# Kernel optimization log

Hardware: AMD Instinct MI355X
Metric: run time of the kernel (lower is better)

The kernel has to match this reference:

```python
import jax, jax.numpy as jnp
import numpy as np

BETA = 0.9
THRESH = 1.0
ALPHA = 2.0  # snntorch ATan surrogate default

@jax.custom_vjp
def atan_spike(x):
    return (x > 0).astype(x.dtype)

def _atan_fwd(x):
    return atan_spike(x), x

def _atan_bwd(x, g):
    # d/dx of snntorch ATan surrogate: (alpha/2) / (1 + (pi/2*alpha*x)^2)
    return (g * (ALPHA / 2) / (1 + (jnp.pi / 2 * ALPHA * x) ** 2),)

atan_spike.defvjp(_atan_fwd, _atan_bwd)

def setup_inputs() -> dict:
    key = jax.random.key(0)
    k1, k2, k3, k4, k5 = jax.random.split(key, 5)
    B, T, F, H, O = 256, 1024, 64, 512, 64
    x = jax.random.normal(k1, (B, T, F), dtype=jnp.float32)
    s_in = 1.0 / np.sqrt(F)
    s_out = 1.0 / np.sqrt(H)
    W_in = jax.random.uniform(k2, (H, F), jnp.float32, -s_in, s_in)
    b_in = jax.random.uniform(k3, (H,), jnp.float32, -s_in, s_in)
    W_out = jax.random.uniform(k4, (O, H), jnp.float32, -s_out, s_out)
    b_out = jax.random.uniform(k5, (O,), jnp.float32, -s_out, s_out)
    return {"x": x, "W_in": W_in, "b_in": b_in, "W_out": W_out, "b_out": b_out}

def reference(x, W_in, b_in, W_out, b_out):
    B, T, F = x.shape
    H = W_in.shape[0]
    O = W_out.shape[0]
    dt = x.dtype
    # precompute input currents for all steps: [T, B, H]
    cur1_all = jnp.einsum('btf,hf->tbh', x, W_in) + b_in

    def step(carry, cur1):
        mem1, mem_out = carry
        # snntorch Leaky(subtract): reset from previous mem (detached),
        # then mem = beta*mem + input - reset*threshold, spike from new mem.
        reset1 = jax.lax.stop_gradient((mem1 > THRESH).astype(dt))
        mem1 = BETA * mem1 + cur1 - reset1 * THRESH
        spk1 = atan_spike(mem1 - THRESH)
        cur_out = spk1 @ W_out.T + b_out
        reset_o = jax.lax.stop_gradient((mem_out > THRESH).astype(dt))
        mem_out = BETA * mem_out + cur_out - reset_o * THRESH
        spk_out = atan_spike(mem_out - THRESH)
        return (mem1, mem_out), (mem_out, spk_out)

    init = (jnp.zeros((B, H), dt), jnp.zeros((B, O), dt))
    _, (mem_rec, spk_rec) = jax.lax.scan(step, init, cur1_all)
    # [T, B, O] -> [B, T, O]
    return mem_rec.transpose(1, 0, 2), spk_rec.transpose(1, 0, 2)
```

## Files before the change

kernel.cpp:

```cpp
#include <hip/hip_runtime.h>


namespace {
constexpr int kB = 256;
constexpr int kT = 1024;
constexpr int kF = 64;
constexpr int kH = 512;
constexpr int kO = 64;
constexpr float kBeta = 0.9f;
constexpr float kThresh = 1.0f;
}

typedef __attribute__((ext_vector_type(16))) float f32x16;

#define PIN8(p)                                                            \
  asm volatile("" : "+v"((p)[0]), "+v"((p)[1]), "+v"((p)[2]),              \
                    "+v"((p)[3]), "+v"((p)[4]), "+v"((p)[5]),              \
                    "+v"((p)[6]), "+v"((p)[7]))

#define BARRIER() asm volatile("s_waitcnt lgkmcnt(0)\n\ts_barrier" ::: "memory")

#define SX(i) ((i) < 16 ? sx0[(i)] : (i) < 32 ? sx1[(i)-16]                \
             : (i) < 48 ? sx2[(i)-32] : sx3[(i)-48])
#define AQ(q)                                                              \
  c0 = fmaf(SX(4*(q)+0), w[4*(q)+0], c0);                                  \
  c1 = fmaf(SX(4*(q)+1), w[4*(q)+1], c1);                                  \
  c2 = fmaf(SX(4*(q)+2), w[4*(q)+2], c2);                                  \
  c3 = fmaf(SX(4*(q)+3), w[4*(q)+3], c3);

__global__ __launch_bounds__(512)
void snn_curA(const float* __restrict__ x, const float* __restrict__ W_in,
              const float* __restrict__ b_in, float* __restrict__ cur1,
              int t0, int ntc, int l2ntc, int rpb) {
  const int l = threadIdx.x & 63;
  const int s = threadIdx.x >> 6;
  const int h = s * 64 + l;

  float w[64];
  {
    const float4* wiv = reinterpret_cast<const float4*>(W_in) + h * 16;
#pragma unroll
    for (int q = 0; q < 16; ++q) {
      const float4 v = wiv[q];
      w[4*q+0] = v.x; w[4*q+1] = v.y; w[4*q+2] = v.z; w[4*q+3] = v.w;
    }
  }
  float binh = b_in[h];
  PIN8(w + 0);  PIN8(w + 8);  PIN8(w + 16); PIN8(w + 24);
  PIN8(w + 32); PIN8(w + 40); PIN8(w + 48); PIN8(w + 56);
  asm volatile("" : "+v"(binh));

  const int row0 = blockIdx.x * rpb;
#pragma unroll 1
  for (int r = 0; r < rpb; ++r) {
    const int row = row0 + r;
    const int b = row >> l2ntc;
    const int tc = row & (ntc - 1);
    const float* xp = x + ((size_t)b * kT + (size_t)(t0 + tc)) * kF;
    f32x16 sx0, sx1, sx2, sx3;
    asm volatile("s_load_dwordx16 %0, %4, 0x0\n\t"
                 "s_load_dwordx16 %1, %4, 0x40\n\t"
                 "s_load_dwordx16 %2, %4, 0x80\n\t"
                 "s_load_dwordx16 %3, %4, 0xc0"
                 : "=&s"(sx0), "=&s"(sx1), "=&s"(sx2), "=&s"(sx3)
                 : "s"(xp));
    asm volatile("s_waitcnt lgkmcnt(0)"
                 : "+s"(sx0), "+s"(sx1), "+s"(sx2), "+s"(sx3) :: "memory");
    float c0 = binh, c1 = 0.0f, c2 = 0.0f, c3 = 0.0f;
    AQ(0) AQ(1) AQ(2) AQ(3) AQ(4) AQ(5) AQ(6) AQ(7)
    AQ(8) AQ(9) AQ(10) AQ(11) AQ(12) AQ(13) AQ(14) AQ(15)
    cur1[(size_t)row * kH + h] = (c0 + c1) + (c2 + c3);
  }
}

#define BSTEP(fk, tt)                                                      \
  do {                                                                     \
    mem1 = kBeta * mem1 + (fk) - rst1;                                     \
    const bool pr = mem1 > kThresh;                                        \
    rst1 = pr ? 1.0f : 0.0f;                                               \
    cp[(size_t)(tt) * kH] = rst1;          \
    const int tn_ = ((tt) + 8 < ntc) ? (tt) + 8 : ntc - 1;                 \
    fk = cp[(size_t)tn_ * kH];         \
  } while (0)

__global__ __launch_bounds__(512)
void snn_scanB(float* __restrict__ cs, float* __restrict__ state,
               int t0, int ntc) {
  const int b = blockIdx.x;
  const int h = threadIdx.x;
  float* m1s = state;
  float* r1s = state + kB * kH;
  const int idx = b * kH + h;
  float mem1 = 0.0f, rst1 = 0.0f;
  if (t0 != 0) { mem1 = m1s[idx]; rst1 = r1s[idx]; }

  float* cp = cs + (size_t)b * ntc * kH + h;
  float f0 = cp[0 * (size_t)kH], f1 = cp[1 * (size_t)kH];
  float f2 = cp[2 * (size_t)kH], f3 = cp[3 * (size_t)kH];
  float f4 = cp[4 * (size_t)kH], f5 = cp[5 * (size_t)kH];
  float f6 = cp[6 * (size_t)kH], f7 = cp[7 * (size_t)kH];

#pragma unroll 1
  for (int t = 0; t < ntc; t += 8) {
    BSTEP(f0, t + 0); BSTEP(f1, t + 1); BSTEP(f2, t + 2); BSTEP(f3, t + 3);
    BSTEP(f4, t + 4); BSTEP(f5, t + 5); BSTEP(f6, t + 6); BSTEP(f7, t + 7);
  }
  m1s[idx] = mem1;
  r1s[idx] = rst1;
}

#define SPK(vv, k)                                                         \
  __int_as_float(__builtin_amdgcn_readlane(__float_as_int(vv), (k)))

#define CROW(vv, rr)                                                       \
  do {                                                                     \
    float a0 = 0.0f, a1 = 0.0f, a2 = 0.0f, a3 = 0.0f;                      \
    _Pragma("unroll") for (int q = 0; q < 16; ++q) {                       \
      a0 = fmaf(SPK(vv, 4 * q + 0), wout[4 * q + 0], a0);                  \
      a1 = fmaf(SPK(vv, 4 * q + 1), wout[4 * q + 1], a1);                  \
      a2 = fmaf(SPK(vv, 4 * q + 2), wout[4 * q + 2], a2);                  \
      a3 = fmaf(SPK(vv, 4 * q + 3), wout[4 * q + 3], a3);                  \
    }                                                                      \
    red[buf][rr][s][o] = (a0 + a1) + (a2 + a3);                            \
  } while (0)

__global__ __launch_bounds__(512)
void snn_coutC(const float* __restrict__ spk, const float* __restrict__ W_out,
               const float* __restrict__ b_out, float* __restrict__ cout,
               int ntc) {
  const int j = threadIdx.x;
  const int o = j & 63;
  const int s = j >> 6;
  const size_t row0 = (size_t)blockIdx.x * 64;

  __shared__ float red[2][8][8][64];

  float wout[64];
  {
    const float4* wov =
        reinterpret_cast<const float4*>(W_out) + o * (kH / 4) + s * 16;
#pragma unroll
    for (int q = 0; q < 16; ++q) {
      const float4 v = wov[q];
      wout[4*q+0] = v.x; wout[4*q+1] = v.y;
      wout[4*q+2] = v.z; wout[4*q+3] = v.w;
    }
  }
  float bout = b_out[o];
  PIN8(wout + 0);  PIN8(wout + 8);  PIN8(wout + 16); PIN8(wout + 24);
  PIN8(wout + 32); PIN8(wout + 40); PIN8(wout + 48); PIN8(wout + 56);
  asm volatile("" : "+v"(bout));

  const float* sb = spk + row0 * kH + j;

#pragma unroll 1
  for (int rb = 0; rb < 64; rb += 8) {
    const int buf = (rb >> 3) & 1;
    float p0 = sb[(size_t)(rb + 0) * kH], p1 = sb[(size_t)(rb + 1) * kH];
    float p2 = sb[(size_t)(rb + 2) * kH], p3 = sb[(size_t)(rb + 3) * kH];
    float p4 = sb[(size_t)(rb + 4) * kH], p5 = sb[(size_t)(rb + 5) * kH];
    float p6 = sb[(size_t)(rb + 6) * kH], p7 = sb[(size_t)(rb + 7) * kH];

    CROW(p0, 0); CROW(p1, 1); CROW(p2, 2); CROW(p3, 3);
    CROW(p4, 4); CROW(p5, 5); CROW(p6, 6); CROW(p7, 7);

    BARRIER();

    float co = bout;
    co += red[buf][s][0][o]; co += red[buf][s][1][o];
    co += red[buf][s][2][o]; co += red[buf][s][3][o];
    co += red[buf][s][4][o]; co += red[buf][s][5][o];
    co += red[buf][s][6][o]; co += red[buf][s][7][o];
    cout[(row0 + (size_t)(rb + s)) * kO + o] = co;
  }
}

#define DSTEP(gk, tt)                                                      \
  do {                                                                     \
    memo = kBeta * memo + (gk) - rsto;                                     \
    const float so = (memo > kThresh) ? 1.0f : 0.0f;                       \
    rsto = so;                                                             \
    om[(size_t)(tt) * kO] = memo;                                          \
    os[(size_t)(tt) * kO] = so;                                            \
    const int tn_ = ((tt) + 8 < ntc) ? (tt) + 8 : ntc - 1;                 \
    gk = dp[(size_t)tn_ * kO];                                             \
  } while (0)

__global__ __launch_bounds__(64)
void snn_memoD(const float* __restrict__ cout, float* __restrict__ out,
               float* __restrict__ state, int t0, int ntc) {
  const int b = blockIdx.x;
  const int o = threadIdx.x;
  float* mos = state + 2 * kB * kH;
  float* ros = mos + kB * kO;
  const int idx = b * kO + o;
  float memo = 0.0f, rsto = 0.0f;
  if (t0 != 0) { memo = mos[idx]; rsto = ros[idx]; }

  const float* dp = cout + (size_t)b * ntc * kO + o;
  float* om = out + ((size_t)b * kT + t0) * kO + o;
  float* os = om + (size_t)kB * kT * kO;

  float g0 = dp[0 * (size_t)kO], g1 = dp[1 * (size_t)kO];
  float g2 = dp[2 * (size_t)kO], g3 = dp[3 * (size_t)kO];
  float g4 = dp[4 * (size_t)kO], g5 = dp[5 * (size_t)kO];
  float g6 = dp[6 * (size_t)kO], g7 = dp[7 * (size_t)kO];

#pragma unroll 1
  for (int t = 0; t < ntc; t += 8) {
    DSTEP(g0, t + 0); DSTEP(g1, t + 1); DSTEP(g2, t + 2); DSTEP(g3, t + 3);
    DSTEP(g4, t + 4); DSTEP(g5, t + 5); DSTEP(g6, t + 6); DSTEP(g7, t + 7);
  }
  mos[idx] = memo;
  ros[idx] = rsto;
}

__global__ __launch_bounds__(256)
void warm_x_kernel(const float4* __restrict__ p, int n4) {
  float acc = 0.0f;
  for (int i = blockIdx.x * blockDim.x + threadIdx.x; i < n4;
       i += gridDim.x * blockDim.x) {
    const float4 v = p[i];
    acc += v.x + v.y + v.z + v.w;
  }
  asm volatile("" ::"v"(acc));
}

__global__ __launch_bounds__(512)
__attribute__((amdgpu_waves_per_eu(2, 2)))
void snn_fused5(const float* __restrict__ x, const float* __restrict__ W_in,
                const float* __restrict__ b_in,
                const float* __restrict__ W_out,
                const float* __restrict__ b_out, float* __restrict__ out) {
  const int b = blockIdx.x;
  const int j = threadIdx.x;
  const int o = j & 63;
  const int s = j >> 6;
  __shared__ float red[2][8][64];
  float win[kF];
  {
    const float4* wiv = reinterpret_cast<const float4*>(W_in) + j * 16;
#pragma unroll
    for (int q = 0; q < 16; ++q) {
      const float4 v = wiv[q];
      win[4 * q] = v.x; win[4 * q + 1] = v.y;
      win[4 * q + 2] = v.z; win[4 * q + 3] = v.w;
    }
  }
  float wout[64];
  {
    const float4* wov =
        reinterpret_cast<const float4*>(W_out) + o * 128 + s * 16;
#pragma unroll
    for (int q = 0; q < 16; ++q) {
      const float4 v = wov[q];
      wout[4 * q] = v.x; wout[4 * q + 1] = v.y;
      wout[4 * q + 2] = v.z; wout[4 * q + 3] = v.w;
    }
  }
  float bin_j = b_in[j];
  float bout_o = b_out[o];
  PIN8(win + 0);  PIN8(win + 8);  PIN8(win + 16); PIN8(win + 24);
  PIN8(win + 32); PIN8(win + 40); PIN8(win + 48); PIN8(win + 56);
  PIN8(wout + 0);  PIN8(wout + 8);  PIN8(wout + 16); PIN8(wout + 24);
  PIN8(wout + 32); PIN8(wout + 40); PIN8(wout + 48); PIN8(wout + 56);
  asm volatile("" : "+v"(bin_j), "+v"(bout_o));
  float mem1 = 0.0f, rst1 = 0.0f, memo = 0.0f, rsto = 0.0f;
  unsigned long long mask = 0ull;
  const float4* xv = reinterpret_cast<const float4*>(x + (size_t)b * kT * kF);
  float* out_mem = out + (size_t)b * kT * kO + o;
  float* out_spk = out_mem + (size_t)kB * kT * kO;
  float4 x0, x1, x2, x3, x4, x5, x6, x7, x8, x9, x10, x11, x12, x13, x14, x15;
#define LOADX(tt)                                                          \
  do {                                                                     \
    const float4* xp = xv + (size_t)(tt) * 16;                             \
    x0 = xp[0]; x1 = xp[1]; x2 = xp[2]; x3 = xp[3];                        \
    x4 = xp[4]; x5 = xp[5]; x6 = xp[6]; x7 = xp[7];                        \
    x8 = xp[8]; x9 = xp[9]; x10 = xp[10]; x11 = xp[11];                    \
    x12 = xp[12]; x13 = xp[13]; x14 = xp[14]; x15 = xp[15];                \
  } while (0)
#define L1Q(q)                                                             \
  c0 = fmaf(x##q.x, win[4 * q + 0], c0);                                   \
  c1 = fmaf(x##q.y, win[4 * q + 1], c1);                                   \
  c2 = fmaf(x##q.z, win[4 * q + 2], c2);                                   \
  c3 = fmaf(x##q.w, win[4 * q + 3], c3);
#define LAYER1F()                                                          \
  do {                                                                     \
    float c0 = bin_j, c1 = 0.0f, c2 = 0.0f, c3 = 0.0f;                     \
    L1Q(0) L1Q(1) L1Q(2) L1Q(3) L1Q(4) L1Q(5) L1Q(6) L1Q(7)                \
    L1Q(8) L1Q(9) L1Q(10) L1Q(11) L1Q(12) L1Q(13) L1Q(14) L1Q(15)          \
    const float cur1v = (c0 + c1) + (c2 + c3);                             \
    mem1 = kBeta * mem1 + cur1v - rst1;                                    \
    const bool p = mem1 > kThresh;                                         \
    mask = __ballot(p);                                                    \
    rst1 = p ? 1.0f : 0.0f;                                                \
  } while (0)
#define L2QS(q)                                                            \
  {                                                                        \
    const float f0 = ((mlo >> (4 * (q) + 0)) & 1u) ? 1.0f : 0.0f;          \
    const float f1 = ((mlo >> (4 * (q) + 1)) & 1u) ? 1.0f : 0.0f;          \
    const float f2 = ((mlo >> (4 * (q) + 2)) & 1u) ? 1.0f : 0.0f;          \
    const float f3 = ((mlo >> (4 * (q) + 3)) & 1u) ? 1.0f : 0.0f;          \
    a0 = fmaf(f0, wout[4 * (q) + 0], a0);                                  \
    a1 = fmaf(f1, wout[4 * (q) + 1], a1);                                  \
    a2 = fmaf(f2, wout[4 * (q) + 2], a2);                                  \
    a3 = fmaf(f3, wout[4 * (q) + 3], a3);                                  \
  }
#define L2E(acc, q, i)                                                     \
  acc = acc + __uint_as_float(                                             \
      (unsigned)__builtin_amdgcn_sbfe((int)vmhi, 4 * (q) + (i)-32, 1) &    \
      __float_as_uint(wout[4 * (q) + (i)]));
#define L2QV(q)                                                            \
  { L2E(a0, q, 0) L2E(a1, q, 1) L2E(a2, q, 2) L2E(a3, q, 3) }
#define LAYER2F(buf)                                                       \
  do {                                                                     \
    const unsigned mlo = (unsigned)mask;                                   \
    unsigned vmhi = (unsigned)(mask >> 32);                                \
    asm volatile("" : "+v"(vmhi));                                         \
    float a0 = 0.0f, a1 = 0.0f, a2 = 0.0f, a3 = 0.0f;                      \
    L2QS(0) L2QS(1) L2QS(2) L2QS(3) L2QS(4) L2QS(5) L2QS(6) L2QS(7)        \
    L2QV(8) L2QV(9) L2QV(10) L2QV(11) L2QV(12) L2QV(13) L2QV(14) L2QV(15)  \
    red[(buf)][s][o] = (a0 + a1) + (a2 + a3);                              \
  } while (0)
  LOADX(0);
  LAYER1F();
  LOADX(1);
  for (int t = 1; t < kT; ++t) {
    LAYER2F((t - 1) & 1);
    BARRIER();
    float r0, r1, r2, r3, r4, r5, r6, r7;
    const int buf = (t - 1) & 1;
    if (s == 0) {
      r0 = red[buf][0][o]; r1 = red[buf][1][o];
      r2 = red[buf][2][o]; r3 = red[buf][3][o];
      r4 = red[buf][4][o]; r5 = red[buf][5][o];
      r6 = red[buf][6][o]; r7 = red[buf][7][o];
    }
    LAYER1F();
    const int tn = (t + 1 < kT) ? (t + 1) : (kT - 1);
    LOADX(tn);
    if (s == 0) {
      float co = bout_o;
      co += r0; co += r1; co += r2; co += r3;
      co += r4; co += r5; co += r6; co += r7;
      memo = kBeta * memo + co - rsto;
      const float so = (memo > kThresh) ? 1.0f : 0.0f;
      rsto = so;
      out_mem[(t - 1) * kO] = memo;
      out_spk[(t - 1) * kO] = so;
    }
  }
  LAYER2F((kT - 1) & 1);
  BARRIER();
  if (s == 0) {
    const int buf = (kT - 1) & 1;
    float co = bout_o;
    co += red[buf][0][o]; co += red[buf][1][o];
    co += red[buf][2][o]; co += red[buf][3][o];
    co += red[buf][4][o]; co += red[buf][5][o];
    co += red[buf][6][o]; co += red[buf][7][o];
    memo = kBeta * memo + co - rsto;
    const float so = (memo > kThresh) ? 1.0f : 0.0f;
    out_mem[(kT - 1) * kO] = memo;
    out_spk[(kT - 1) * kO] = so;
  }
}

extern "C" void kernel_launch(void* const* d_in, const int* in_sizes, int n_in,
                              void* d_out, int out_size, void* d_ws,
                              size_t ws_size, hipStream_t stream) {
  const float* x = (const float*)d_in[0];
  const float* W_in = (const float*)d_in[1];
  const float* b_in = (const float*)d_in[2];
  const float* W_out = (const float*)d_in[3];
  const float* b_out = (const float*)d_in[4];
  float* out = (float*)d_out;

  const size_t state_bytes = ((size_t)2 * kB * kH + 2 * kB * kO) * 4;
  int nch = 0;
  for (int c : {4, 8, 16}) {
    const int ntc_c = kT / c;
    const size_t need = (size_t)kB * ntc_c * (kH + kO) * 4 + state_bytes;
    if (need <= ws_size) { nch = c; break; }
  }

  if (nch) {
    const int ntc = kT / nch;
    const int l2ntc = (ntc == 256) ? 8 : (ntc == 128) ? 7 : 6;
    float* cur1 = (float*)d_ws;
    float* coutb = cur1 + (size_t)kB * ntc * kH;
    float* state = coutb + (size_t)kB * ntc * kO;

    const int rows = kB * ntc;
    const int rpbA = 128;
    const int gA = rows / rpbA;
    const int gC = rows / 64;

    for (int c = 0; c < nch; ++c) {
      const int t0 = c * ntc;
      hipLaunchKernelGGL(snn_curA, dim3(gA), dim3(512), 0, stream,
                         x, W_in, b_in, cur1, t0, ntc, l2ntc, rpbA);
      hipLaunchKernelGGL(snn_scanB, dim3(kB), dim3(512), 0, stream,
                         cur1, state, t0, ntc);
      hipLaunchKernelGGL(snn_coutC, dim3(gC), dim3(512), 0, stream,
                         cur1, W_out, b_out, coutb, ntc);
      hipLaunchKernelGGL(snn_memoD, dim3(kB), dim3(64), 0, stream,
                         coutb, out, state, t0, ntc);
    }
  } else {
    const int n4 = kB * kT * kF / 4;
    hipLaunchKernelGGL(warm_x_kernel, dim3(1024), dim3(256), 0, stream,
                       (const float4*)x, n4);
    hipLaunchKernelGGL(snn_fused5, dim3(kB), dim3(512), 0, stream,
                       x, W_in, b_in, W_out, b_out, out);
  }
}
```

Measured before the change: 1.170 ms.

## Pack hidden spikes into ballot bitmasks and compute two hidden units per thread

The scan kernel no longer writes float spikes back over the cur1 buffer. It emits one 64-bit ballot mask per wave per timestep, and the output-current kernel reads these masks with scalar loads and expands bits into FMAs. This replaces a large float write and read with a much smaller bitmask stream. The input-current kernel now uses 256 threads that each compute two hidden units, halving the scalar x loads per output. Rows per block and chunk count are retuned, and a 2-chunk option is allowed when the workspace fits. The costs are higher register pressure and bit-extraction ALU work.

Measured after the change: 1.587 ms. +35.6%, slower.

```diff
diff --git a/kernel.cpp b/kernel.cpp
--- a/kernel.cpp
+++ b/kernel.cpp
@@ -12,6 +12,7 @@
 }
 
 typedef __attribute__((ext_vector_type(16))) float f32x16;
+typedef __attribute__((ext_vector_type(2))) unsigned int u32x2;
 
 #define PIN8(p)                                                            \
   asm volatile("" : "+v"((p)[0]), "+v"((p)[1]), "+v"((p)[2]),              \
@@ -20,35 +21,55 @@
 
 #define BARRIER() asm volatile("s_waitcnt lgkmcnt(0)\n\ts_barrier" ::: "memory")
 
+#define SLOAD64(sx0, sx1, sx2, sx3, ptr)                                   \
+  asm volatile("s_load_dwordx16 %0, %4, 0x0\n\t"                           \
+               "s_load_dwordx16 %1, %4, 0x40\n\t"                          \
+               "s_load_dwordx16 %2, %4, 0x80\n\t"                          \
+               "s_load_dwordx16 %3, %4, 0xc0\n\t"                          \
+               "s_waitcnt lgkmcnt(0)"                                      \
+               : "=&s"(sx0), "=&s"(sx1), "=&s"(sx2), "=&s"(sx3)            \
+               : "s"(ptr) : "memory")
+
 #define SX(i) ((i) < 16 ? sx0[(i)] : (i) < 32 ? sx1[(i)-16]                \
              : (i) < 48 ? sx2[(i)-32] : sx3[(i)-48])
-#define AQ(q)                                                              \
-  c0 = fmaf(SX(4*(q)+0), w[4*(q)+0], c0);                                  \
-  c1 = fmaf(SX(4*(q)+1), w[4*(q)+1], c1);                                  \
-  c2 = fmaf(SX(4*(q)+2), w[4*(q)+2], c2);                                  \
-  c3 = fmaf(SX(4*(q)+3), w[4*(q)+3], c3);
-
-__global__ __launch_bounds__(512)
+#define AQ2(q)                                                             \
+  c0 = fmaf(SX(4*(q)+0), wA[4*(q)+0], c0);                                 \
+  c1 = fmaf(SX(4*(q)+1), wA[4*(q)+1], c1);                                 \
+  c2 = fmaf(SX(4*(q)+2), wA[4*(q)+2], c2);                                 \
+  c3 = fmaf(SX(4*(q)+3), wA[4*(q)+3], c3);                                 \
+  e0 = fmaf(SX(4*(q)+0), wB[4*(q)+0], e0);                                 \
+  e1 = fmaf(SX(4*(q)+1), wB[4*(q)+1], e1);                                 \
+  e2 = fmaf(SX(4*(q)+2), wB[4*(q)+2], e2);                                 \
+  e3 = fmaf(SX(4*(q)+3), wB[4*(q)+3], e3);
+
+__global__ __launch_bounds__(256)
+__attribute__((amdgpu_waves_per_eu(2, 2)))
 void snn_curA(const float* __restrict__ x, const float* __restrict__ W_in,
               const float* __restrict__ b_in, float* __restrict__ cur1,
               int t0, int ntc, int l2ntc, int rpb) {
   const int l = threadIdx.x & 63;
   const int s = threadIdx.x >> 6;
-  const int h = s * 64 + l;
-
-  float w[64];
+  const int h0 = s * 64 + l;
+  const int h1 = h0 + 256;
+
+  float wA[64], wB[64];
   {
-    const float4* wiv = reinterpret_cast<const float4*>(W_in) + h * 16;
+    const float4* w0 = reinterpret_cast<const float4*>(W_in) + h0 * 16;
+    const float4* w1 = reinterpret_cast<const float4*>(W_in) + h1 * 16;
 #pragma unroll
     for (int q = 0; q < 16; ++q) {
-      const float4 v = wiv[q];
-      w[4*q+0] = v.x; w[4*q+1] = v.y; w[4*q+2] = v.z; w[4*q+3] = v.w;
-    }
-  }
-  float binh = b_in[h];
-  PIN8(w + 0);  PIN8(w + 8);  PIN8(w + 16); PIN8(w + 24);
-  PIN8(w + 32); PIN8(w + 40); PIN8(w + 48); PIN8(w + 56);
-  asm volatile("" : "+v"(binh));
+      const float4 a = w0[q];
+      wA[4*q+0] = a.x; wA[4*q+1] = a.y; wA[4*q+2] = a.z; wA[4*q+3] = a.w;
+      const float4 b = w1[q];
+      wB[4*q+0] = b.x; wB[4*q+1] = b.y; wB[4*q+2] = b.z; wB[4*q+3] = b.w;
+    }
+  }
+  float bin0 = b_in[h0], bin1 = b_in[h1];
+  PIN8(wA + 0);  PIN8(wA + 8);  PIN8(wA + 16); PIN8(wA + 24);
+  PIN8(wA + 32); PIN8(wA + 40); PIN8(wA + 48); PIN8(wA + 56);
+  PIN8(wB + 0);  PIN8(wB + 8);  PIN8(wB + 16); PIN8(wB + 24);
+  PIN8(wB + 32); PIN8(wB + 40); PIN8(wB + 48); PIN8(wB + 56);
+  asm volatile("" : "+v"(bin0), "+v"(bin1));
 
   const int row0 = blockIdx.x * rpb;
 #pragma unroll 1
@@ -58,18 +79,14 @@
     const int tc = row & (ntc - 1);
     const float* xp = x + ((size_t)b * kT + (size_t)(t0 + tc)) * kF;
     f32x16 sx0, sx1, sx2, sx3;
-    asm volatile("s_load_dwordx16 %0, %4, 0x0\n\t"
-                 "s_load_dwordx16 %1, %4, 0x40\n\t"
-                 "s_load_dwordx16 %2, %4, 0x80\n\t"
-                 "s_load_dwordx16 %3, %4, 0xc0"
-                 : "=&s"(sx0), "=&s"(sx1), "=&s"(sx2), "=&s"(sx3)
-                 : "s"(xp));
-    asm volatile("s_waitcnt lgkmcnt(0)"
-                 : "+s"(sx0), "+s"(sx1), "+s"(sx2), "+s"(sx3) :: "memory");
-    float c0 = binh, c1 = 0.0f, c2 = 0.0f, c3 = 0.0f;
-    AQ(0) AQ(1) AQ(2) AQ(3) AQ(4) AQ(5) AQ(6) AQ(7)
-    AQ(8) AQ(9) AQ(10) AQ(11) AQ(12) AQ(13) AQ(14) AQ(15)
-    cur1[(size_t)row * kH + h] = (c0 + c1) + (c2 + c3);
+    SLOAD64(sx0, sx1, sx2, sx3, xp);
+    float c0 = bin0, c1 = 0.0f, c2 = 0.0f, c3 = 0.0f;
+    float e0 = bin1, e1 = 0.0f, e2 = 0.0f, e3 = 0.0f;
+    AQ2(0) AQ2(1) AQ2(2) AQ2(3) AQ2(4) AQ2(5) AQ2(6) AQ2(7)
+    AQ2(8) AQ2(9) AQ2(10) AQ2(11) AQ2(12) AQ2(13) AQ2(14) AQ2(15)
+    float* cb = cur1 + (size_t)row * kH;
+    cb[h0] = (c0 + c1) + (c2 + c3);
+    cb[h1] = (e0 + e1) + (e2 + e3);
   }
 }
 
@@ -77,24 +94,30 @@
   do {                                                                     \
     mem1 = kBeta * mem1 + (fk) - rst1;                                     \
     const bool pr = mem1 > kThresh;                                        \
+    const unsigned long long mk = __ballot(pr);                            \
     rst1 = pr ? 1.0f : 0.0f;                                               \
-    cp[(size_t)(tt) * kH] = rst1;          \
+    if (l == 0)                                                            \
+      *reinterpret_cast<unsigned long long*>(bitp + (size_t)(tt) * 16) = mk; \
     const int tn_ = ((tt) + 8 < ntc) ? (tt) + 8 : ntc - 1;                 \
-    fk = cp[(size_t)tn_ * kH];         \
+    fk = cp[(size_t)tn_ * kH];                                             \
   } while (0)
 
 __global__ __launch_bounds__(512)
-void snn_scanB(float* __restrict__ cs, float* __restrict__ state,
-               int t0, int ntc) {
+void snn_scanB(const float* __restrict__ cs, unsigned int* __restrict__ bits,
+               float* __restrict__ state, int t0, int ntc) {
   const int b = blockIdx.x;
   const int h = threadIdx.x;
+  const int l = h & 63;
+  const int w = h >> 6;
   float* m1s = state;
   float* r1s = state + kB * kH;
   const int idx = b * kH + h;
   float mem1 = 0.0f, rst1 = 0.0f;
   if (t0 != 0) { mem1 = m1s[idx]; rst1 = r1s[idx]; }
 
-  float* cp = cs + (size_t)b * ntc * kH + h;
+  const float* cp = cs + (size_t)b * ntc * kH + h;
+  unsigned int* bitp = bits + (size_t)b * ntc * 16 + w * 2;
+
   float f0 = cp[0 * (size_t)kH], f1 = cp[1 * (size_t)kH];
   float f2 = cp[2 * (size_t)kH], f3 = cp[3 * (size_t)kH];
   float f4 = cp[4 * (size_t)kH], f5 = cp[5 * (size_t)kH];
@@ -109,28 +132,28 @@
   r1s[idx] = rst1;
 }
 
-#define SPK(vv, k)                                                         \
-  __int_as_float(__builtin_amdgcn_readlane(__float_as_int(vv), (k)))
-
-#define CROW(vv, rr)                                                       \
-  do {                                                                     \
-    float a0 = 0.0f, a1 = 0.0f, a2 = 0.0f, a3 = 0.0f;                      \
-    _Pragma("unroll") for (int q = 0; q < 16; ++q) {                       \
-      a0 = fmaf(SPK(vv, 4 * q + 0), wout[4 * q + 0], a0);                  \
-      a1 = fmaf(SPK(vv, 4 * q + 1), wout[4 * q + 1], a1);                  \
-      a2 = fmaf(SPK(vv, 4 * q + 2), wout[4 * q + 2], a2);                  \
-      a3 = fmaf(SPK(vv, 4 * q + 3), wout[4 * q + 3], a3);                  \
-    }                                                                      \
-    red[buf][rr][s][o] = (a0 + a1) + (a2 + a3);                            \
-  } while (0)
+#define FB(m, k) ((((m) >> (k)) & 1u) ? 1.0f : 0.0f)
+#define CQL(q)                                                             \
+  a0 = fmaf(FB(mlo, 4*(q)+0), wout[4*(q)+0], a0);                          \
+  a1 = fmaf(FB(mlo, 4*(q)+1), wout[4*(q)+1], a1);                          \
+  a2 = fmaf(FB(mlo, 4*(q)+2), wout[4*(q)+2], a2);                          \
+  a3 = fmaf(FB(mlo, 4*(q)+3), wout[4*(q)+3], a3);
+#define CQH(q)                                                             \
+  a0 = fmaf(FB(mhi, 4*(q)+0-32), wout[4*(q)+0], a0);                       \
+  a1 = fmaf(FB(mhi, 4*(q)+1-32), wout[4*(q)+1], a1);                       \
+  a2 = fmaf(FB(mhi, 4*(q)+2-32), wout[4*(q)+2], a2);                       \
+  a3 = fmaf(FB(mhi, 4*(q)+3-32), wout[4*(q)+3], a3);
 
 __global__ __launch_bounds__(512)
-void snn_coutC(const float* __restrict__ spk, const float* __restrict__ W_out,
+__attribute__((amdgpu_waves_per_eu(2, 2)))
+void snn_coutC(const unsigned int* __restrict__ bits,
+               const float* __restrict__ W_out,
                const float* __restrict__ b_out, float* __restrict__ cout,
                int ntc) {
   const int j = threadIdx.x;
   const int o = j & 63;
   const int s = j >> 6;
+  const int s_u = __builtin_amdgcn_readfirstlane(s);
   const size_t row0 = (size_t)blockIdx.x * 64;
 
   __shared__ float red[2][8][8][64];
@@ -151,19 +174,25 @@
   PIN8(wout + 32); PIN8(wout + 40); PIN8(wout + 48); PIN8(wout + 56);
   asm volatile("" : "+v"(bout));
 
-  const float* sb = spk + row0 * kH + j;
+  const unsigned int* bitbase = bits + row0 * 16 + s_u * 2;
 
 #pragma unroll 1
   for (int rb = 0; rb < 64; rb += 8) {
     const int buf = (rb >> 3) & 1;
-    float p0 = sb[(size_t)(rb + 0) * kH], p1 = sb[(size_t)(rb + 1) * kH];
-    float p2 = sb[(size_t)(rb + 2) * kH], p3 = sb[(size_t)(rb + 3) * kH];
-    float p4 = sb[(size_t)(rb + 4) * kH], p5 = sb[(size_t)(rb + 5) * kH];
-    float p6 = sb[(size_t)(rb + 6) * kH], p7 = sb[(size_t)(rb + 7) * kH];
-
-    CROW(p0, 0); CROW(p1, 1); CROW(p2, 2); CROW(p3, 3);
-    CROW(p4, 4); CROW(p5, 5); CROW(p6, 6); CROW(p7, 7);
-
+#pragma unroll
+    for (int r = 0; r < 8; ++r) {
+      const unsigned int* bp = bitbase + (size_t)(rb + r) * 16;
+      u32x2 mm;
+      asm volatile("s_load_dwordx2 %0, %1, 0x0\n\t"
+                   "s_waitcnt lgkmcnt(0)"
+                   : "=&s"(mm) : "s"(bp) : "memory");
+      const unsigned int mlo = mm[0];
+      const unsigned int mhi = mm[1];
+      float a0 = 0.0f, a1 = 0.0f, a2 = 0.0f, a3 = 0.0f;
+      CQL(0) CQL(1) CQL(2) CQL(3) CQL(4) CQL(5) CQL(6) CQL(7)
+      CQH(8) CQH(9) CQH(10) CQH(11) CQH(12) CQH(13) CQH(14) CQH(15)
+      red[buf][r][s][o] = (a0 + a1) + (a2 + a3);
+    }
     BARRIER();
 
     float co = bout;
@@ -378,32 +407,36 @@
 
   const size_t state_bytes = ((size_t)2 * kB * kH + 2 * kB * kO) * 4;
   int nch = 0;
-  for (int c : {4, 8, 16}) {
+  for (int c : {2, 4, 8, 16}) {
     const int ntc_c = kT / c;
-    const size_t need = (size_t)kB * ntc_c * (kH + kO) * 4 + state_bytes;
+    const size_t rows_c = (size_t)kB * ntc_c;
+    const size_t need =
+        rows_c * (kH + kO) * 4 + rows_c * 16 * 4 + state_bytes;
     if (need <= ws_size) { nch = c; break; }
   }
 
   if (nch) {
     const int ntc = kT / nch;
-    const int l2ntc = (ntc == 256) ? 8 : (ntc == 128) ? 7 : 6;
+    const int l2ntc = (ntc == 512) ? 9 : (ntc == 256) ? 8
+                     : (ntc == 128) ? 7 : 6;
+    const size_t rows = (size_t)kB * ntc;
     float* cur1 = (float*)d_ws;
-    float* coutb = cur1 + (size_t)kB * ntc * kH;
-    float* state = coutb + (size_t)kB * ntc * kO;
-
-    const int rows = kB * ntc;
-    const int rpbA = 128;
-    const int gA = rows / rpbA;
-    const int gC = rows / 64;
+    float* coutb = cur1 + rows * kH;
+    unsigned int* bitsb = (unsigned int*)(coutb + rows * kO);
+    float* state = (float*)(bitsb + rows * 16);
+
+    const int rpbA = 64;
+    const int gA = (int)(rows / rpbA);
+    const int gC = (int)(rows / 64);
 
     for (int c = 0; c < nch; ++c) {
       const int t0 = c * ntc;
-      hipLaunchKernelGGL(snn_curA, dim3(gA), dim3(512), 0, stream,
+      hipLaunchKernelGGL(snn_curA, dim3(gA), dim3(256), 0, stream,
                          x, W_in, b_in, cur1, t0, ntc, l2ntc, rpbA);
       hipLaunchKernelGGL(snn_scanB, dim3(kB), dim3(512), 0, stream,
-                         cur1, state, t0, ntc);
+                         cur1, bitsb, state, t0, ntc);
       hipLaunchKernelGGL(snn_coutC, dim3(gC), dim3(512), 0, stream,
-                         cur1, W_out, b_out, coutb, ntc);
+                         bitsb, W_out, b_out, coutb, ntc);
       hipLaunchKernelGGL(snn_memoD, dim3(kB), dim3(64), 0, stream,
                          coutb, out, state, t0, ntc);
     }
```
